# Performance work log

Measured on AMD Instinct MI355X. Metric: run time of the kernel, lower is better.

Reference implementation:

```python
import jax, jax.numpy as jnp
import numpy as np

D_MODEL = 1024
STATE_DIM = 64
SEQ_L = 2048


def hippo_legs_A(N):
    n = jnp.arange(N, dtype=jnp.float32)
    two_n1 = 2.0 * n + 1.0
    sq = jnp.sqrt(two_n1[:, None] * two_n1[None, :])
    A = jnp.tril(sq, k=-1) * -1.0
    return A + jnp.diag(-(n + 1.0))


def setup_inputs() -> dict:
    key = jax.random.key(0)
    kB, kC = jax.random.split(key)
    N = STATE_DIM
    n = jnp.arange(N, dtype=jnp.float32)
    B_ref = jnp.sqrt(2.0 * n + 1.0)  # (N,)
    B = jnp.tile(B_ref[None, :], (D_MODEL, 1)) + 0.01 * jax.random.normal(kB, (D_MODEL, N), dtype=jnp.float32)
    C = 0.1 * jax.random.normal(kC, (D_MODEL, N), dtype=jnp.float32)
    D = jnp.zeros((D_MODEL,), dtype=jnp.float32)
    log_dt = jnp.log(jnp.asarray(0.1, dtype=jnp.float32))
    return {"B": B, "C": C, "D": D, "log_dt": log_dt, "L": SEQ_L}


def reference(B, C, D, log_dt, L):
    N = B.shape[1]
    A = hippo_legs_A(N)                       # (N,N) continuous-time HiPPO-LegS
    dt = jax.nn.softplus(log_dt) + 1e-06
    I = jnp.eye(N, dtype=A.dtype)
    lhs = I - 0.5 * dt * A
    rhs = I + 0.5 * dt * A
    A_bar = jnp.linalg.solve(lhs, rhs)        # (N,N) bilinear discretization
    B_bar = jnp.linalg.solve(lhs, (dt * B).T).T  # (d_model, N)
    A_bar_T = A_bar.T

    def step(x, _):
        y = jnp.sum(C * x, axis=-1)           # (d_model,)
        return x @ A_bar_T, y

    _, ys = jax.lax.scan(step, B_bar, None, length=L)  # ys: (L, d_model)
    K = ys.T                                   # (d_model, L)
    K = K.at[:, 0].add(D)
    return K[:, None, :]                       # (d_model, 1, L)
```

## Files before the change

### kernel.cpp

```cpp
#include <hip/hip_runtime.h>

namespace {

template<int CTRL, int RM>
__device__ __forceinline__ float dpp_mov0(float v) {
  return __int_as_float(__builtin_amdgcn_update_dpp(
      0, __float_as_int(v), CTRL, RM, 0xF, false));
}
template<int CTRL, int RM>
__device__ __forceinline__ float dpp_mov1(float v) {
  return __int_as_float(__builtin_amdgcn_update_dpp(
      0x3f800000, __float_as_int(v), CTRL, RM, 0xF, false));
}

__device__ __forceinline__ float scan_add64(float v) {
  v += dpp_mov0<0x111, 0xF>(v);
  v += dpp_mov0<0x112, 0xF>(v);
  v += dpp_mov0<0x114, 0xF>(v);
  v += dpp_mov0<0x118, 0xF>(v);
  v += dpp_mov0<0x142, 0xA>(v);
  v += dpp_mov0<0x143, 0xC>(v);
  return v;
}

template<int CTRL, int RM>
__device__ __forceinline__ void linrec_step(float& G, float& W) {
  float Wo = dpp_mov0<CTRL, RM>(W);
  float Go = dpp_mov1<CTRL, RM>(G);
  W = fmaf(G, Wo, W);
  G *= Go;
}
__device__ __forceinline__ float scan_linrec64(float g, float w) {
  float G = g, W = w;
  linrec_step<0x111, 0xF>(G, W);
  linrec_step<0x112, 0xF>(G, W);
  linrec_step<0x114, 0xF>(G, W);
  linrec_step<0x118, 0xF>(G, W);
  linrec_step<0x142, 0xA>(G, W);
  linrec_step<0x143, 0xC>(G, W);
  return W;
}

struct Coef {
  float r, inv_d, g, hr, tmd;
};

__device__ __forceinline__ Coef make_coef(float dt, int n) {
  Coef c;
  float h = 0.5f * dt;
  float fn = (float)n;
  c.r = sqrtf(2.f * fn + 1.f);
  float dc = 1.f + h * (fn + 1.f);
  c.inv_d = 1.f / dc;
  c.g = (1.f - h * fn) / dc;
  c.hr = h * c.r;
  c.tmd = 2.f - dc;
  return c;
}

__device__ __forceinline__ float lhs_solve(float z, const Coef& c, int lane) {
  float W = scan_linrec64(c.g, c.r * z * c.inv_d);
  float sp = __shfl_up(W, 1, 64);
  if (lane == 0) sp = 0.f;
  return (z - c.hr * sp) * c.inv_d;
}

__device__ __forceinline__ float abar_apply(float x, const Coef& c, int lane) {
  float t = c.r * x;
  float S = scan_add64(t);
  float Sp = S - t;
  float z = c.tmd * x - c.hr * Sp;
  return lhs_solve(z, c, lane);
}

__device__ __forceinline__ float softplus_dt(float ldt) {
  return log1pf(expf(ldt)) + 1e-6f;
}

}

__global__ __launch_bounds__(64) void hippo_pow64(const float* __restrict__ ldt_p,
                                                  float* __restrict__ PT) {
  const int lane = threadIdx.x;
  const int m = blockIdx.x;
  const float dt = softplus_dt(ldt_p[0]);
  const Coef c = make_coef(dt, lane);
  float x = (lane == m) ? 1.f : 0.f;
  for (int s = 0; s < 64; ++s) x = abar_apply(x, c, lane);
  PT[m * 64 + lane] = x;
}

__global__ __launch_bounds__(256) void hippo_main(
    const float* __restrict__ B, const float* __restrict__ C,
    const float* __restrict__ Dv, const float* __restrict__ ldt_p,
    const float* __restrict__ PT, float* __restrict__ out, int NI, int L) {
  __shared__ __align__(16) float Vl[64 * 65];
  __shared__ __align__(16) float Ul[32 * 64];
  const int d = blockIdx.x;
  const int tau = threadIdx.x;
  const int lane = tau & 63;
  const int w = tau >> 6;
  const float dt = softplus_dt(ldt_p[0]);
  const Coef c = make_coef(dt, lane);

  if (w == 0) {
    float b = B[d * 64 + lane];
    float v = lhs_solve(dt * b, c, lane);
    for (int j = 0; j < 64; ++j) {
      Vl[j * 65 + lane] = v;
      if (j < 63) v = abar_apply(v, c, lane);
    }
  } else if (w == 1) {
    float pc[64];
    const float4* pt4 = (const float4*)(PT + lane * 64);
    #pragma unroll
    for (int q = 0; q < 16; ++q) {
      float4 f = pt4[q];
      pc[4*q+0] = f.x; pc[4*q+1] = f.y; pc[4*q+2] = f.z; pc[4*q+3] = f.w;
    }
    float u = C[d * 64 + lane];
    for (int i = 0; i < NI; ++i) {
      Ul[i * 64 + lane] = u;
      if (i < NI - 1) {
        float a0 = 0.f, a1 = 0.f, a2 = 0.f, a3 = 0.f;
        #pragma unroll
        for (int k = 0; k < 64; k += 4) {
          float u0 = __int_as_float(__builtin_amdgcn_readlane(__float_as_int(u), k + 0));
          float u1 = __int_as_float(__builtin_amdgcn_readlane(__float_as_int(u), k + 1));
          float u2 = __int_as_float(__builtin_amdgcn_readlane(__float_as_int(u), k + 2));
          float u3 = __int_as_float(__builtin_amdgcn_readlane(__float_as_int(u), k + 3));
          a0 = fmaf(pc[k+0], u0, a0);
          a1 = fmaf(pc[k+1], u1, a1);
          a2 = fmaf(pc[k+2], u2, a2);
          a3 = fmaf(pc[k+3], u3, a3);
        }
        u = (a0 + a1) + (a2 + a3);
      }
    }
  }
  __syncthreads();

  const int j = lane;
  float vr[64];
  #pragma unroll
  for (int n = 0; n < 64; ++n) vr[n] = Vl[j * 65 + n];
  for (int i = w; i < NI; i += 4) {
    const float4* u4 = (const float4*)(Ul + i * 64);
    float a0 = 0.f, a1 = 0.f, a2 = 0.f, a3 = 0.f;
    #pragma unroll
    for (int q = 0; q < 16; ++q) {
      float4 f = u4[q];
      a0 = fmaf(vr[4*q+0], f.x, a0);
      a1 = fmaf(vr[4*q+1], f.y, a1);
      a2 = fmaf(vr[4*q+2], f.z, a2);
      a3 = fmaf(vr[4*q+3], f.w, a3);
    }
    float y = (a0 + a1) + (a2 + a3);
    if ((i | j) == 0) y += Dv[d];
    out[(size_t)d * L + i * 64 + j] = y;
  }
}

extern "C" void kernel_launch(void* const* d_in, const int* in_sizes, int n_in,
                              void* d_out, int out_size, void* d_ws, size_t ws_size,
                              hipStream_t stream) {
  const float* B   = (const float*)d_in[0];
  const float* C   = (const float*)d_in[1];
  const float* Dv  = (const float*)d_in[2];
  const float* ldt = (const float*)d_in[3];
  const int d_model = in_sizes[2];
  const int L = out_size / d_model;
  const int NI = L / 64;
  float* PT = (float*)d_ws;
  hippo_pow64<<<64, 64, 0, stream>>>(ldt, PT);
  hippo_main<<<d_model, 256, 0, stream>>>(B, C, Dv, ldt, PT, (float*)d_out, NI, L);
}
```

Measured before the change: 40.82 us.

## Split C-side power chain into even/odd streams and fuse A_bar apply scans

Adds a kernel that precomputes the squared 64-step propagator (Q2 = P^2), so two wavefronts generate the even and odd blocks of C-side vectors in parallel, halving the serial chain length in the main kernel. The A_bar apply is rewritten to fold the prefix-sum and linear-recurrence solve into a single fused DPP scan, and a DPP row shift replaces the shuffle. The final dot-product phase is restructured to load V in two halves of 32 registers to reduce register pressure. The cost is an extra small kernel launch plus extra workspace.

```diff
diff --git a/kernel.cpp b/kernel.cpp
--- a/kernel.cpp
+++ b/kernel.cpp
@@ -13,14 +13,46 @@
       0x3f800000, __float_as_int(v), CTRL, RM, 0xF, false));
 }
 
-__device__ __forceinline__ float scan_add64(float v) {
-  v += dpp_mov0<0x111, 0xF>(v);
-  v += dpp_mov0<0x112, 0xF>(v);
-  v += dpp_mov0<0x114, 0xF>(v);
-  v += dpp_mov0<0x118, 0xF>(v);
-  v += dpp_mov0<0x142, 0xA>(v);
-  v += dpp_mov0<0x143, 0xC>(v);
-  return v;
+struct Coef {
+  float r, inv_d, hr, g0, c0, alpha, k2;
+};
+
+__device__ __forceinline__ Coef make_coef(float dt, int n) {
+  float h = 0.5f * dt, fn = (float)n;
+  float r = sqrtf(2.f * fn + 1.f);
+  float d = 1.f + h * (fn + 1.f);
+  float inv_d = 1.f / d;
+  float g0 = (1.f - h * fn) * inv_d;
+  Coef c;
+  c.r = r; c.inv_d = inv_d; c.hr = h * r;
+  c.g0 = g0; c.c0 = g0 - 1.f;
+  c.alpha = 1.f + h * fn;
+  c.k2 = r * (2.f - d) * inv_d;
+  return c;
+}
+
+template<int CTRL, int RM>
+__device__ __forceinline__ void fused_step(float& c, float& g, float& w1, float& w2) {
+  float cP  = dpp_mov0<CTRL, RM>(c);
+  float gP  = dpp_mov1<CTRL, RM>(g);
+  float w1P = dpp_mov0<CTRL, RM>(w1);
+  float w2P = dpp_mov0<CTRL, RM>(w2);
+  w2 = fmaf(g, w2P, fmaf(c, w1P, w2));
+  c  = fmaf(g, cP, c);
+  g  = g * gP;
+  w1 = w1 + w1P;
+}
+
+__device__ __forceinline__ float abar_apply(float x, const Coef& c) {
+  float cc = c.c0, g = c.g0, w1 = c.r * x, w2 = c.k2 * x;
+  fused_step<0x111, 0xF>(cc, g, w1, w2);
+  fused_step<0x112, 0xF>(cc, g, w1, w2);
+  fused_step<0x114, 0xF>(cc, g, w1, w2);
+  fused_step<0x118, 0xF>(cc, g, w1, w2);
+  fused_step<0x142, 0xA>(cc, g, w1, w2);
+  fused_step<0x143, 0xC>(cc, g, w1, w2);
+  float tp = dpp_mov0<0x138, 0xF>(w2);
+  return c.inv_d * fmaf(-c.hr, w1 + tp, c.alpha * x);
 }
 
 template<int CTRL, int RM>
@@ -30,51 +62,45 @@
   W = fmaf(G, Wo, W);
   G *= Go;
 }
-__device__ __forceinline__ float scan_linrec64(float g, float w) {
-  float G = g, W = w;
+__device__ __forceinline__ float lhs_solve(float z, const Coef& c) {
+  float G = c.g0, W = c.r * z * c.inv_d;
   linrec_step<0x111, 0xF>(G, W);
   linrec_step<0x112, 0xF>(G, W);
   linrec_step<0x114, 0xF>(G, W);
   linrec_step<0x118, 0xF>(G, W);
   linrec_step<0x142, 0xA>(G, W);
   linrec_step<0x143, 0xC>(G, W);
-  return W;
-}
-
-struct Coef {
-  float r, inv_d, g, hr, tmd;
-};
-
-__device__ __forceinline__ Coef make_coef(float dt, int n) {
-  Coef c;
-  float h = 0.5f * dt;
-  float fn = (float)n;
-  c.r = sqrtf(2.f * fn + 1.f);
-  float dc = 1.f + h * (fn + 1.f);
-  c.inv_d = 1.f / dc;
-  c.g = (1.f - h * fn) / dc;
-  c.hr = h * c.r;
-  c.tmd = 2.f - dc;
-  return c;
-}
-
-__device__ __forceinline__ float lhs_solve(float z, const Coef& c, int lane) {
-  float W = scan_linrec64(c.g, c.r * z * c.inv_d);
-  float sp = __shfl_up(W, 1, 64);
-  if (lane == 0) sp = 0.f;
+  float sp = dpp_mov0<0x138, 0xF>(W);
   return (z - c.hr * sp) * c.inv_d;
-}
-
-__device__ __forceinline__ float abar_apply(float x, const Coef& c, int lane) {
-  float t = c.r * x;
-  float S = scan_add64(t);
-  float Sp = S - t;
-  float z = c.tmd * x - c.hr * Sp;
-  return lhs_solve(z, c, lane);
 }
 
 __device__ __forceinline__ float softplus_dt(float ldt) {
   return log1pf(expf(ldt)) + 1e-6f;
+}
+
+__device__ __forceinline__ float qapply(const float (&pc)[64], float u) {
+  float a0 = 0.f, a1 = 0.f, a2 = 0.f, a3 = 0.f;
+  #pragma unroll
+  for (int k = 0; k < 64; k += 4) {
+    float u0 = __int_as_float(__builtin_amdgcn_readlane(__float_as_int(u), k + 0));
+    float u1 = __int_as_float(__builtin_amdgcn_readlane(__float_as_int(u), k + 1));
+    float u2 = __int_as_float(__builtin_amdgcn_readlane(__float_as_int(u), k + 2));
+    float u3 = __int_as_float(__builtin_amdgcn_readlane(__float_as_int(u), k + 3));
+    a0 = fmaf(pc[k + 0], u0, a0);
+    a1 = fmaf(pc[k + 1], u1, a1);
+    a2 = fmaf(pc[k + 2], u2, a2);
+    a3 = fmaf(pc[k + 3], u3, a3);
+  }
+  return (a0 + a1) + (a2 + a3);
+}
+
+__device__ __forceinline__ void load_row(const float* __restrict__ base, float (&pc)[64]) {
+  const float4* p4 = (const float4*)base;
+  #pragma unroll
+  for (int q = 0; q < 16; ++q) {
+    float4 f = p4[q];
+    pc[4*q+0] = f.x; pc[4*q+1] = f.y; pc[4*q+2] = f.z; pc[4*q+3] = f.w;
+  }
 }
 
 }
@@ -86,14 +112,26 @@
   const float dt = softplus_dt(ldt_p[0]);
   const Coef c = make_coef(dt, lane);
   float x = (lane == m) ? 1.f : 0.f;
-  for (int s = 0; s < 64; ++s) x = abar_apply(x, c, lane);
+  for (int s = 0; s < 64; ++s) x = abar_apply(x, c);
   PT[m * 64 + lane] = x;
+}
+
+__global__ __launch_bounds__(64) void hippo_q2(const float* __restrict__ PT,
+                                               float* __restrict__ Q2) {
+  const int lane = threadIdx.x;
+  const int m = blockIdx.x;
+  float pc[64];
+  load_row(PT + lane * 64, pc);
+  float u = PT[lane * 64 + m];
+  float v = qapply(pc, u);
+  Q2[lane * 64 + m] = v;
 }
 
 __global__ __launch_bounds__(256) void hippo_main(
     const float* __restrict__ B, const float* __restrict__ C,
     const float* __restrict__ Dv, const float* __restrict__ ldt_p,
-    const float* __restrict__ PT, float* __restrict__ out, int NI, int L) {
+    const float* __restrict__ PT, const float* __restrict__ Q2,
+    float* __restrict__ out, int NI, int L) {
   __shared__ __align__(16) float Vl[64 * 65];
   __shared__ __align__(16) float Ul[32 * 64];
   const int d = blockIdx.x;
@@ -104,60 +142,69 @@
   const Coef c = make_coef(dt, lane);
 
   if (w == 0) {
-    float b = B[d * 64 + lane];
-    float v = lhs_solve(dt * b, c, lane);
+    float v = lhs_solve(dt * B[d * 64 + lane], c);
     for (int j = 0; j < 64; ++j) {
       Vl[j * 65 + lane] = v;
-      if (j < 63) v = abar_apply(v, c, lane);
+      if (j < 63) v = abar_apply(v, c);
     }
   } else if (w == 1) {
     float pc[64];
-    const float4* pt4 = (const float4*)(PT + lane * 64);
+    load_row(Q2 + lane * 64, pc);
+    float u = C[d * 64 + lane];
+    const int nE = (NI + 1) >> 1;
+    for (int a = 0; a < nE; ++a) {
+      Ul[(2 * a) * 64 + lane] = u;
+      if (a < nE - 1) u = qapply(pc, u);
+    }
+  } else if (w == 2) {
+    float pc[64];
+    load_row(PT + lane * 64, pc);
+    float u = C[d * 64 + lane];
+    u = qapply(pc, u);
+    load_row(Q2 + lane * 64, pc);
+    const int nO = NI >> 1;
+    for (int a = 0; a < nO; ++a) {
+      Ul[(2 * a + 1) * 64 + lane] = u;
+      if (a < nO - 1) u = qapply(pc, u);
+    }
+  }
+  __syncthreads();
+
+  const int j = lane;
+  float acc[8];
+  #pragma unroll
+  for (int k = 0; k < 8; ++k) acc[k] = 0.f;
+  #pragma unroll
+  for (int h = 0; h < 2; ++h) {
+    float vr[32];
     #pragma unroll
-    for (int q = 0; q < 16; ++q) {
-      float4 f = pt4[q];
-      pc[4*q+0] = f.x; pc[4*q+1] = f.y; pc[4*q+2] = f.z; pc[4*q+3] = f.w;
-    }
-    float u = C[d * 64 + lane];
-    for (int i = 0; i < NI; ++i) {
-      Ul[i * 64 + lane] = u;
-      if (i < NI - 1) {
+    for (int n = 0; n < 32; ++n) vr[n] = Vl[j * 65 + h * 32 + n];
+    #pragma unroll
+    for (int k = 0; k < 8; ++k) {
+      const int i = w + 4 * k;
+      if (i < NI) {
+        const float4* u4 = (const float4*)(Ul + i * 64 + h * 32);
         float a0 = 0.f, a1 = 0.f, a2 = 0.f, a3 = 0.f;
         #pragma unroll
-        for (int k = 0; k < 64; k += 4) {
-          float u0 = __int_as_float(__builtin_amdgcn_readlane(__float_as_int(u), k + 0));
-          float u1 = __int_as_float(__builtin_amdgcn_readlane(__float_as_int(u), k + 1));
-          float u2 = __int_as_float(__builtin_amdgcn_readlane(__float_as_int(u), k + 2));
-          float u3 = __int_as_float(__builtin_amdgcn_readlane(__float_as_int(u), k + 3));
-          a0 = fmaf(pc[k+0], u0, a0);
-          a1 = fmaf(pc[k+1], u1, a1);
-          a2 = fmaf(pc[k+2], u2, a2);
-          a3 = fmaf(pc[k+3], u3, a3);
+        for (int q = 0; q < 8; ++q) {
+          float4 f = u4[q];
+          a0 = fmaf(vr[4*q+0], f.x, a0);
+          a1 = fmaf(vr[4*q+1], f.y, a1);
+          a2 = fmaf(vr[4*q+2], f.z, a2);
+          a3 = fmaf(vr[4*q+3], f.w, a3);
         }
-        u = (a0 + a1) + (a2 + a3);
+        acc[k] += (a0 + a1) + (a2 + a3);
       }
     }
   }
-  __syncthreads();
-
-  const int j = lane;
-  float vr[64];
-  #pragma unroll
-  for (int n = 0; n < 64; ++n) vr[n] = Vl[j * 65 + n];
-  for (int i = w; i < NI; i += 4) {
-    const float4* u4 = (const float4*)(Ul + i * 64);
-    float a0 = 0.f, a1 = 0.f, a2 = 0.f, a3 = 0.f;
-    #pragma unroll
-    for (int q = 0; q < 16; ++q) {
-      float4 f = u4[q];
-      a0 = fmaf(vr[4*q+0], f.x, a0);
-      a1 = fmaf(vr[4*q+1], f.y, a1);
-      a2 = fmaf(vr[4*q+2], f.z, a2);
-      a3 = fmaf(vr[4*q+3], f.w, a3);
-    }
-    float y = (a0 + a1) + (a2 + a3);
-    if ((i | j) == 0) y += Dv[d];
-    out[(size_t)d * L + i * 64 + j] = y;
+  #pragma unroll
+  for (int k = 0; k < 8; ++k) {
+    const int i = w + 4 * k;
+    if (i < NI) {
+      float y = acc[k];
+      if ((i | j) == 0) y += Dv[d];
+      out[(size_t)d * L + i * 64 + j] = y;
+    }
   }
 }
 
@@ -172,6 +219,8 @@
   const int L = out_size / d_model;
   const int NI = L / 64;
   float* PT = (float*)d_ws;
+  float* Q2 = (float*)d_ws + 64 * 64;
   hippo_pow64<<<64, 64, 0, stream>>>(ldt, PT);
-  hippo_main<<<d_model, 256, 0, stream>>>(B, C, Dv, ldt, PT, (float*)d_out, NI, L);
-}
+  hippo_q2<<<64, 64, 0, stream>>>(PT, Q2);
+  hippo_main<<<d_model, 256, 0, stream>>>(B, C, Dv, ldt, PT, Q2, (float*)d_out, NI, L);
+}
```

Result: slower. 54.65 us (+33.9%).
